# Kernel tuning notes

Hardware: AMD Instinct MI355X
Metric: run time of the kernel (lower is better)

Reference implementation:

```python
import jax, jax.numpy as jnp
import numpy as np

T, B, I, H = 4096, 64, 128, 128


def setup_inputs() -> dict:
    key = jax.random.key(0)
    k1, k2, k3, k4, k5 = jax.random.split(key, 5)
    s = 1.0 / np.sqrt(H)
    return {
        "x": jax.random.normal(k1, (T, B, I), dtype=jnp.float32),
        "h0": jnp.zeros((B, H), dtype=jnp.float32),
        "W_ih": jax.random.normal(k2, (H, I), dtype=jnp.float32) * s,
        "W_hh": jax.random.normal(k3, (H, H), dtype=jnp.float32) * s,
        "b_ih": jax.random.normal(k4, (H,), dtype=jnp.float32) * s,
        "b_hh": jax.random.normal(k5, (H,), dtype=jnp.float32) * s,
    }


def reference(x, h0, W_ih, W_hh, b_ih, b_hh):
    # Precompute the input projection for all timesteps in one big GEMM
    # (mathematically identical to per-step x_t @ W_ih^T).
    xp = jnp.einsum("tbi,hi->tbh", x, W_ih) + b_ih  # [T, B, H]

    def step(h, xp_t):
        h = jnp.tanh(xp_t + h @ W_hh.T + b_hh)
        return h, h

    h_final, hs = jax.lax.scan(step, h0, xp)  # hs: [T, B, H]
    return hs, h_final[None]
```

## Files before the change

kernel.cpp:

```cpp
#include <hip/hip_runtime.h>

#define T_N 4096
#define B_N 64
#define I_N 128
#define H_N 128
#define BH  (B_N * H_N)

__global__ __launch_bounds__(256) void xproj_kernel(
    const float* __restrict__ x, const float* __restrict__ Wih,
    const float* __restrict__ bih, float* __restrict__ xp)
{
    __shared__ float wt[I_N][H_N];
    const int tid = threadIdx.x;

    {
        const float4* w4 = (const float4*)Wih;
        #pragma unroll
        for (int it = 0; it < 16; ++it) {
            int i = tid * 16 + it;
            float4 v = w4[i];
            int r = i >> 5;
            int k = (i & 31) << 2;
            wt[k + 0][r] = v.x;
            wt[k + 1][r] = v.y;
            wt[k + 2][r] = v.z;
            wt[k + 3][r] = v.w;
        }
    }
    __syncthreads();

    const int  tx   = tid & 15;
    const int  ty   = tid >> 4;
    const long row0 = (long)blockIdx.x * 128;
    const float* xbase = x + (row0 + ty * 8) * I_N;

    float acc[8][8];
    #pragma unroll
    for (int r = 0; r < 8; ++r)
        #pragma unroll
        for (int c = 0; c < 8; ++c) acc[r][c] = 0.0f;

    #pragma unroll 2
    for (int k4 = 0; k4 < I_N / 4; ++k4) {
        float4 xv[8];
        #pragma unroll
        for (int r = 0; r < 8; ++r)
            xv[r] = *(const float4*)(xbase + r * I_N + k4 * 4);

        #pragma unroll
        for (int kk = 0; kk < 4; ++kk) {
            int k = k4 * 4 + kk;
            float4 w0 = *(const float4*)&wt[k][tx * 4];
            float4 w1 = *(const float4*)&wt[k][64 + tx * 4];
            #pragma unroll
            for (int r = 0; r < 8; ++r) {
                float xk = (kk == 0) ? xv[r].x : (kk == 1) ? xv[r].y
                         : (kk == 2) ? xv[r].z : xv[r].w;
                acc[r][0] = fmaf(xk, w0.x, acc[r][0]);
                acc[r][1] = fmaf(xk, w0.y, acc[r][1]);
                acc[r][2] = fmaf(xk, w0.z, acc[r][2]);
                acc[r][3] = fmaf(xk, w0.w, acc[r][3]);
                acc[r][4] = fmaf(xk, w1.x, acc[r][4]);
                acc[r][5] = fmaf(xk, w1.y, acc[r][5]);
                acc[r][6] = fmaf(xk, w1.z, acc[r][6]);
                acc[r][7] = fmaf(xk, w1.w, acc[r][7]);
            }
        }
    }

    float4 b0 = *(const float4*)(bih + tx * 4);
    float4 b1 = *(const float4*)(bih + 64 + tx * 4);
    #pragma unroll
    for (int r = 0; r < 8; ++r) {
        long row = row0 + ty * 8 + r;
        float4 o0, o1;
        o0.x = acc[r][0] + b0.x;  o0.y = acc[r][1] + b0.y;
        o0.z = acc[r][2] + b0.z;  o0.w = acc[r][3] + b0.w;
        o1.x = acc[r][4] + b1.x;  o1.y = acc[r][5] + b1.y;
        o1.z = acc[r][6] + b1.z;  o1.w = acc[r][7] + b1.w;
        *(float4*)(xp + row * H_N + tx * 4)      = o0;
        *(float4*)(xp + row * H_N + 64 + tx * 4) = o1;
    }
}

__device__ __forceinline__ float tanh_pade(float x) {
    float u = x * x;
    float n = fmaf(u, u + 105.0f, 945.0f);
    float d = fmaf(u, fmaf(15.0f, u, 420.0f), 945.0f);
    float t = x * n * __builtin_amdgcn_rcpf(d);
    return fminf(1.0f, fmaxf(-1.0f, t));
}

#define DPP_XOR1 0xB1

__device__ __forceinline__ float dpp_add_xor1(float v) {
    int s = __float_as_int(v);
    int r = __builtin_amdgcn_update_dpp(0, s, DPP_XOR1, 0xF, 0xF, true);
    return v + __int_as_float(r);
}

#define DOT4(W4, H4)                                                          \
    fmaf((W4).x, (H4).x, fmaf((W4).y, (H4).y,                                 \
    fmaf((W4).z, (H4).z, (W4).w * (H4).w)))

__global__ __launch_bounds__(256, 1) void scan_kernel(
    const float* __restrict__ Whh, const float* __restrict__ bhh,
    const float* __restrict__ h0, float* __restrict__ out)
{
    const int tid  = threadIdx.x;
    const int b    = blockIdx.x;
    const int lane = tid & 63;
    const int wv   = tid >> 6;
    const int p    = lane & 1;
    const int j    = (lane >> 1) + 32 * wv;
    __shared__ float hbuf[2][2][68];

    float4 w[16];
    #pragma unroll
    for (int c = 0; c < 16; ++c)
        w[c] = *(const float4*)(Whh + j * H_N + 64 * p + 4 * c);

    const float bh = bhh[j];

    if (tid < H_N) hbuf[0][tid >> 6][tid & 63] = h0[b * H_N + tid];

    const float* xq = out + b * H_N + j;
    float*       oq = out + b * H_N + j;

    float xv[4];
    #pragma unroll
    for (int d = 0; d < 4; ++d)
        xv[d] = xq[(size_t)d * BH];

    __syncthreads();

#define RNN_STEP(T0, D, CUR) do {                                             \
        const float4* hb = (const float4*)&hbuf[CUR][p][0];                   \
        float4 hv0 = hb[0],  hv1 = hb[1],  hv2 = hb[2],  hv3 = hb[3];         \
        float4 hv4 = hb[4],  hv5 = hb[5],  hv6 = hb[6],  hv7 = hb[7];         \
        float4 hv8 = hb[8],  hv9 = hb[9],  hvA = hb[10], hvB = hb[11];        \
        float4 hvC = hb[12], hvD = hb[13], hvE = hb[14], hvF = hb[15];        \
        float d0 = DOT4(w[0],  hv0) + DOT4(w[1],  hv1);                       \
        float d1 = DOT4(w[2],  hv2) + DOT4(w[3],  hv3);                       \
        float d2 = DOT4(w[4],  hv4) + DOT4(w[5],  hv5);                       \
        float d3 = DOT4(w[6],  hv6) + DOT4(w[7],  hv7);                       \
        float d4 = DOT4(w[8],  hv8) + DOT4(w[9],  hv9);                       \
        float d5 = DOT4(w[10], hvA) + DOT4(w[11], hvB);                       \
        float d6 = DOT4(w[12], hvC) + DOT4(w[13], hvD);                       \
        float d7 = DOT4(w[14], hvE) + DOT4(w[15], hvF);                       \
        float s = ((d0 + d1) + (d2 + d3)) + ((d4 + d5) + (d6 + d7));          \
        s = dpp_add_xor1(s);                                                  \
        if (p == 0) {                                                         \
            float hj = tanh_pade(s + xv[D] + bh);                             \
            hbuf[(CUR) ^ 1][j >> 6][j & 63] = hj;                             \
            oq[(size_t)(T0) * BH] = hj;                                       \
            if ((T0) == T_N - 1) oq[(size_t)T_N * BH] = hj;                   \
        }                                                                     \
        if ((T0) + 4 < T_N)                                                   \
            xv[D] = xq[(size_t)((T0) + 4) * BH];                              \
        asm volatile("s_waitcnt lgkmcnt(0)" ::: "memory");                    \
        __builtin_amdgcn_s_barrier();                                         \
        asm volatile("" ::: "memory");                                        \
    } while (0)

    for (int t = 0; t < T_N; t += 4) {
        RNN_STEP(t + 0, 0, 0);
        RNN_STEP(t + 1, 1, 1);
        RNN_STEP(t + 2, 2, 0);
        RNN_STEP(t + 3, 3, 1);
    }
#undef RNN_STEP
}

extern "C" void kernel_launch(void* const* d_in, const int* in_sizes, int n_in,
                              void* d_out, int out_size, void* d_ws, size_t ws_size,
                              hipStream_t stream) {
    const float* x   = (const float*)d_in[0];
    const float* h0  = (const float*)d_in[1];
    const float* Wih = (const float*)d_in[2];
    const float* Whh = (const float*)d_in[3];
    const float* bih = (const float*)d_in[4];
    const float* bhh = (const float*)d_in[5];
    float* out = (float*)d_out;

    xproj_kernel<<<dim3((T_N * B_N) / 128), 256, 0, stream>>>(x, Wih, bih, out);
    scan_kernel<<<dim3(B_N), 256, 0, stream>>>(Whh, bhh, h0, out);
}
```

Measured before the change: 1.689 ms.

## Run recurrent scan on fp16 MFMA with 16 batches per block

Replaces the per-batch scalar FMA dot-product scan with a matrix-core version. Each block handles 16 batch rows, and each of 8 waves computes a 16x128 slice of W_hh·h with four 16x16x32 fp16 MFMAs per step. The hidden state lives in fp16 shared memory. This cuts the serial per-step compute and moves the scan from 64 blocks to 4. In exchange it adds fp16 rounding to the recurrent state and weights and uses far fewer CUs.

Result: faster. 1.555 ms (-8.0%).

```diff
diff --git a/kernel.cpp b/kernel.cpp
--- a/kernel.cpp
+++ b/kernel.cpp
@@ -5,6 +5,12 @@
 #define I_N 128
 #define H_N 128
 #define BH  (B_N * H_N)
+#define NB2 16
+#define NPAD 136
+
+typedef _Float16 half8 __attribute__((ext_vector_type(8)));
+typedef _Float16 half4 __attribute__((ext_vector_type(4)));
+typedef float    f32x4 __attribute__((ext_vector_type(4)));
 
 __global__ __launch_bounds__(256) void xproj_kernel(
     const float* __restrict__ x, const float* __restrict__ Wih,
@@ -91,85 +97,86 @@
     return fminf(1.0f, fmaxf(-1.0f, t));
 }
 
-#define DPP_XOR1 0xB1
-
-__device__ __forceinline__ float dpp_add_xor1(float v) {
-    int s = __float_as_int(v);
-    int r = __builtin_amdgcn_update_dpp(0, s, DPP_XOR1, 0xF, 0xF, true);
-    return v + __int_as_float(r);
-}
-
-#define DOT4(W4, H4)                                                          \
-    fmaf((W4).x, (H4).x, fmaf((W4).y, (H4).y,                                 \
-    fmaf((W4).z, (H4).z, (W4).w * (H4).w)))
-
-__global__ __launch_bounds__(256, 1) void scan_kernel(
+__global__ __launch_bounds__(512, 1) void scan_mfma(
     const float* __restrict__ Whh, const float* __restrict__ bhh,
     const float* __restrict__ h0, float* __restrict__ out)
 {
     const int tid  = threadIdx.x;
-    const int b    = blockIdx.x;
     const int lane = tid & 63;
     const int wv   = tid >> 6;
-    const int p    = lane & 1;
-    const int j    = (lane >> 1) + 32 * wv;
-    __shared__ float hbuf[2][2][68];
+    const int r16  = lane & 15;
+    const int kg   = lane >> 4;
+    const int jb   = wv * 16;
+    const int b    = blockIdx.x * NB2 + r16;
 
-    float4 w[16];
+    __shared__ __align__(16) _Float16 hbuf[2][NB2][NPAD];
+
+    half8 afrag[4];
     #pragma unroll
-    for (int c = 0; c < 16; ++c)
-        w[c] = *(const float4*)(Whh + j * H_N + 64 * p + 4 * c);
+    for (int m = 0; m < 4; ++m) {
+        const float* wp = Whh + (size_t)(jb + r16) * H_N + m * 32 + kg * 8;
+        float4 wa = *(const float4*)wp;
+        float4 wb = *(const float4*)(wp + 4);
+        afrag[m][0] = (_Float16)wa.x; afrag[m][1] = (_Float16)wa.y;
+        afrag[m][2] = (_Float16)wa.z; afrag[m][3] = (_Float16)wa.w;
+        afrag[m][4] = (_Float16)wb.x; afrag[m][5] = (_Float16)wb.y;
+        afrag[m][6] = (_Float16)wb.z; afrag[m][7] = (_Float16)wb.w;
+    }
 
-    const float bh = bhh[j];
+    const float4 bh4 = *(const float4*)(bhh + jb + 4 * kg);
 
-    if (tid < H_N) hbuf[0][tid >> 6][tid & 63] = h0[b * H_N + tid];
+    for (int i = tid; i < NB2 * H_N; i += 512) {
+        int bt = i >> 7, j = i & 127;
+        hbuf[0][bt][j] = (_Float16)h0[(size_t)(blockIdx.x * NB2 + bt) * H_N + j];
+    }
 
-    const float* xq = out + b * H_N + j;
-    float*       oq = out + b * H_N + j;
+    const float* xq = out + (size_t)b * H_N + jb + 4 * kg;
+    float*       oq = out + (size_t)b * H_N + jb + 4 * kg;
 
-    float xv[4];
+    float4 xv[4];
     #pragma unroll
     for (int d = 0; d < 4; ++d)
-        xv[d] = xq[(size_t)d * BH];
+        xv[d] = *(const float4*)(xq + (size_t)d * BH);
 
     __syncthreads();
 
-#define RNN_STEP(T0, D, CUR) do {                                             \
-        const float4* hb = (const float4*)&hbuf[CUR][p][0];                   \
-        float4 hv0 = hb[0],  hv1 = hb[1],  hv2 = hb[2],  hv3 = hb[3];         \
-        float4 hv4 = hb[4],  hv5 = hb[5],  hv6 = hb[6],  hv7 = hb[7];         \
-        float4 hv8 = hb[8],  hv9 = hb[9],  hvA = hb[10], hvB = hb[11];        \
-        float4 hvC = hb[12], hvD = hb[13], hvE = hb[14], hvF = hb[15];        \
-        float d0 = DOT4(w[0],  hv0) + DOT4(w[1],  hv1);                       \
-        float d1 = DOT4(w[2],  hv2) + DOT4(w[3],  hv3);                       \
-        float d2 = DOT4(w[4],  hv4) + DOT4(w[5],  hv5);                       \
-        float d3 = DOT4(w[6],  hv6) + DOT4(w[7],  hv7);                       \
-        float d4 = DOT4(w[8],  hv8) + DOT4(w[9],  hv9);                       \
-        float d5 = DOT4(w[10], hvA) + DOT4(w[11], hvB);                       \
-        float d6 = DOT4(w[12], hvC) + DOT4(w[13], hvD);                       \
-        float d7 = DOT4(w[14], hvE) + DOT4(w[15], hvF);                       \
-        float s = ((d0 + d1) + (d2 + d3)) + ((d4 + d5) + (d6 + d7));          \
-        s = dpp_add_xor1(s);                                                  \
-        if (p == 0) {                                                         \
-            float hj = tanh_pade(s + xv[D] + bh);                             \
-            hbuf[(CUR) ^ 1][j >> 6][j & 63] = hj;                             \
-            oq[(size_t)(T0) * BH] = hj;                                       \
-            if ((T0) == T_N - 1) oq[(size_t)T_N * BH] = hj;                   \
-        }                                                                     \
+#define STEP(T0, D, CUR, NXT) do {                                            \
+        const _Float16* hb = &hbuf[CUR][r16][0];                              \
+        half8 bf0 = *(const half8*)(hb + kg * 8);                             \
+        half8 bf1 = *(const half8*)(hb + 32 + kg * 8);                        \
+        half8 bf2 = *(const half8*)(hb + 64 + kg * 8);                        \
+        half8 bf3 = *(const half8*)(hb + 96 + kg * 8);                        \
+        f32x4 acc0 = {0.f, 0.f, 0.f, 0.f};                                    \
+        f32x4 acc1 = {0.f, 0.f, 0.f, 0.f};                                    \
+        acc0 = __builtin_amdgcn_mfma_f32_16x16x32_f16(afrag[0], bf0, acc0, 0, 0, 0); \
+        acc1 = __builtin_amdgcn_mfma_f32_16x16x32_f16(afrag[1], bf1, acc1, 0, 0, 0); \
+        acc0 = __builtin_amdgcn_mfma_f32_16x16x32_f16(afrag[2], bf2, acc0, 0, 0, 0); \
+        acc1 = __builtin_amdgcn_mfma_f32_16x16x32_f16(afrag[3], bf3, acc1, 0, 0, 0); \
+        float4 hv;                                                            \
+        hv.x = tanh_pade(acc0[0] + acc1[0] + xv[D].x + bh4.x);                \
+        hv.y = tanh_pade(acc0[1] + acc1[1] + xv[D].y + bh4.y);                \
+        hv.z = tanh_pade(acc0[2] + acc1[2] + xv[D].z + bh4.z);                \
+        hv.w = tanh_pade(acc0[3] + acc1[3] + xv[D].w + bh4.w);                \
+        half4 hh;                                                             \
+        hh[0] = (_Float16)hv.x; hh[1] = (_Float16)hv.y;                       \
+        hh[2] = (_Float16)hv.z; hh[3] = (_Float16)hv.w;                       \
+        *(half4*)&hbuf[NXT][r16][jb + 4 * kg] = hh;                           \
+        *(float4*)(oq + (size_t)(T0) * BH) = hv;                              \
+        if ((T0) == T_N - 1) *(float4*)(oq + (size_t)T_N * BH) = hv;          \
         if ((T0) + 4 < T_N)                                                   \
-            xv[D] = xq[(size_t)((T0) + 4) * BH];                              \
+            xv[D] = *(const float4*)(xq + (size_t)((T0) + 4) * BH);           \
         asm volatile("s_waitcnt lgkmcnt(0)" ::: "memory");                    \
         __builtin_amdgcn_s_barrier();                                         \
         asm volatile("" ::: "memory");                                        \
     } while (0)
 
     for (int t = 0; t < T_N; t += 4) {
-        RNN_STEP(t + 0, 0, 0);
-        RNN_STEP(t + 1, 1, 1);
-        RNN_STEP(t + 2, 2, 0);
-        RNN_STEP(t + 3, 3, 1);
+        STEP(t + 0, 0, 0, 1);
+        STEP(t + 1, 1, 1, 0);
+        STEP(t + 2, 2, 0, 1);
+        STEP(t + 3, 3, 1, 0);
     }
-#undef RNN_STEP
+#undef STEP
 }
 
 extern "C" void kernel_launch(void* const* d_in, const int* in_sizes, int n_in,
@@ -184,5 +191,5 @@
     float* out = (float*)d_out;
 
     xproj_kernel<<<dim3((T_N * B_N) / 128), 256, 0, stream>>>(x, Wih, bih, out);
-    scan_kernel<<<dim3(B_N), 256, 0, stream>>>(Whh, bhh, h0, out);
+    scan_mfma<<<dim3(B_N / NB2), 512, 0, stream>>>(Whh, bhh, h0, out);
 }
```
